# Kernel tuning notes

Measured on AMD Instinct MI355X. Metric: run time of the kernel, lower is better.

The kernel has to match this reference:

```python
import jax, jax.numpy as jnp
import numpy as np

CROP_SIZE = (14, 14)
NUM_LEVELS = 5
CANONICAL_SIZE = 224.0
CANONICAL_LEVEL = 1.0
EPS = 1e-7  # keras.backend.epsilon()


def _map_to_level(boxes):
    # boxes: [N, 4] (x1, y1, x2, y2) in image pixels
    w = boxes[:, 2] - boxes[:, 0]
    h = boxes[:, 3] - boxes[:, 1]
    size = jnp.sqrt(w * h)
    lv = jnp.floor(CANONICAL_LEVEL + jnp.log2(size / CANONICAL_SIZE + EPS))
    return jnp.clip(lv, 0.0, NUM_LEVELS - 1.0)


def _crop_and_resize(img, boxes, crop_size):
    # TF tf.image.crop_and_resize semantics (bilinear, extrapolation_value=0).
    # img: [H, W, C]; boxes: [N, 4] normalized (y1, x1, y2, x2)
    H, W, _ = img.shape
    ch, cw = crop_size
    y1, x1, y2, x2 = boxes[:, 0], boxes[:, 1], boxes[:, 2], boxes[:, 3]
    ty = jnp.arange(ch, dtype=boxes.dtype) / (ch - 1)
    tx = jnp.arange(cw, dtype=boxes.dtype) / (cw - 1)
    ys = (y1[:, None] * (1 - ty) + y2[:, None] * ty) * (H - 1)  # [N, ch]
    xs = (x1[:, None] * (1 - tx) + x2[:, None] * tx) * (W - 1)  # [N, cw]

    def corners(c, size):
        lo = jnp.floor(c)
        frac = c - lo
        lo_i = jnp.clip(lo, 0, size - 1).astype(jnp.int32)
        hi_i = jnp.clip(lo + 1, 0, size - 1).astype(jnp.int32)
        valid = (c >= 0) & (c <= size - 1)
        return lo_i, hi_i, frac, valid

    y0, y1i, fy, vy = corners(ys, H)
    x0, x1i, fx, vx = corners(xs, W)
    # gather 4 corners: [N, ch, cw, C]
    tl = img[y0[:, :, None], x0[:, None, :]]
    tr = img[y0[:, :, None], x1i[:, None, :]]
    bl = img[y1i[:, :, None], x0[:, None, :]]
    br = img[y1i[:, :, None], x1i[:, None, :]]
    fxb = fx[:, None, :, None]
    fyb = fy[:, :, None, None]
    top = tl + (tr - tl) * fxb
    bot = bl + (br - bl) * fxb
    out = top + (bot - top) * fyb
    mask = (vy[:, :, None] & vx[:, None, :])[:, :, :, None]
    return jnp.where(mask, out, 0.0)


def _roi_align(image_shape, boxes, scores, fpn):
    img_h = image_shape[1].astype(jnp.float32)
    img_w = image_shape[2].astype(jnp.float32)
    levels = _map_to_level(boxes)
    x1b, y1b, x2b, y2b = boxes[:, 0], boxes[:, 1], boxes[:, 2], boxes[:, 3]
    out = jnp.zeros((boxes.shape[0], CROP_SIZE[0], CROP_SIZE[1], fpn[0].shape[-1]),
                    dtype=fpn[0].dtype)
    for i, f in enumerate(fpn):
        fh = jnp.float32(f.shape[0])
        fw = jnp.float32(f.shape[1])
        # exact box normalization from the keras module
        nb = jnp.stack([
            y1b / img_h * fh / (fh - 1),
            x1b / img_w * fw / (fw - 1),
            (y2b / img_h * fh - 1) / (fh - 1),
            (x2b / img_w * fw - 1) / (fw - 1)], axis=1)
        crop = _crop_and_resize(f, nb, CROP_SIZE)
        sel = (levels == i)[:, None, None, None]
        # per-box level routing (equivalent to gather -> crop -> scatter_nd)
        out = out + jnp.where(sel, crop, 0.0)
    return out[None]  # [1, N, ch, cw, C]


def setup_inputs() -> dict:
    key = jax.random.key(0)
    ks = jax.random.split(key, 10)
    N, C, IMG = 512, 256, 1024.0
    cx = jax.random.uniform(ks[0], (N,), minval=16.0, maxval=IMG - 16.0)
    cy = jax.random.uniform(ks[1], (N,), minval=16.0, maxval=IMG - 16.0)
    # log-uniform box sizes 16..512 px so all 5 FPN levels are populated
    sz = jnp.exp(jax.random.uniform(ks[2], (N,), minval=jnp.log(16.0), maxval=jnp.log(512.0)))
    ar = jnp.exp(jax.random.uniform(ks[3], (N,), minval=jnp.log(0.5), maxval=jnp.log(2.0)))
    w = sz * jnp.sqrt(ar)
    h = sz / jnp.sqrt(ar)
    x1 = jnp.clip(cx - w / 2, 0.0, IMG)
    x2 = jnp.clip(cx + w / 2, 0.0, IMG)
    y1 = jnp.clip(cy - h / 2, 0.0, IMG)
    y2 = jnp.clip(cy + h / 2, 0.0, IMG)
    boxes = jnp.stack([x1, y1, x2, y2], axis=1)[None]  # [1, N, 4]
    scores = jax.random.uniform(ks[4], (1, N), dtype=jnp.float32)
    sizes = [256, 128, 64, 32, 16]  # FPN strides 4..64 on a 1024px image
    fpn = {f"fpn{i}": jax.random.normal(ks[5 + i], (1, s, s, C), dtype=jnp.float32)
           for i, s in enumerate(sizes)}
    return {"image_shape": jnp.array([1, 1024, 1024, 3], dtype=jnp.int32),
            "boxes": boxes, "scores": scores, **fpn}


def reference(image_shape, boxes, scores, fpn0, fpn1, fpn2, fpn3, fpn4):
    b = jax.lax.stop_gradient(boxes[0])
    s = jax.lax.stop_gradient(scores[0])
    fpn = [jax.lax.stop_gradient(f[0]) for f in (fpn0, fpn1, fpn2, fpn3, fpn4)]
    return _roi_align(image_shape, b, s, fpn)
```

## Files before the change

kernel.cpp:

```cpp
#include <hip/hip_runtime.h>


#define CROP 14
#define POS (CROP * CROP)
#define C 256
#define CANON 224.0f
#define EPSF 1e-7f
#define PPW 4
#define BLK_PER_BOX 13

typedef float vfloat4 __attribute__((ext_vector_type(4)));

__global__ __launch_bounds__(256) void roi_align_kernel(
    const int* __restrict__ image_shape,
    const float* __restrict__ boxes,
    const float* __restrict__ f0,
    const float* __restrict__ f1,
    const float* __restrict__ f2,
    const float* __restrict__ f3,
    const float* __restrict__ f4,
    float* __restrict__ out)
{
    const int nwg = gridDim.x;
    const int q = nwg >> 3, r = nwg & 7;
    const int xcd = blockIdx.x & 7, slot = blockIdx.x >> 3;
    const int blk = (xcd < r ? xcd * (q + 1) : r * (q + 1) + (xcd - r) * q) + slot;

    const int box      = blk / BLK_PER_BOX;
    const int blkInBox = blk % BLK_PER_BOX;
    const int wave = threadIdx.x >> 6;
    const int lane = threadIdx.x & 63;
    const int pbase = (blkInBox * 4 + wave) * PPW;

    const float imgh = (float)image_shape[1];
    const float imgw = (float)image_shape[2];

    const float bx1 = boxes[box * 4 + 0];
    const float by1 = boxes[box * 4 + 1];
    const float bx2 = boxes[box * 4 + 2];
    const float by2 = boxes[box * 4 + 3];

    const float w  = bx2 - bx1;
    const float h  = by2 - by1;
    const float sz = sqrtf(w * h);
    float lvf = floorf(1.0f + log2f(sz / CANON + EPSF));
    lvf = fminf(fmaxf(lvf, 0.0f), 4.0f);
    const int lv = (int)lvf;

    const int   s  = 256 >> lv;
    const float fh = (float)s;
    const float fw = (float)s;

    const float ny1 = by1 / imgh * fh / (fh - 1.0f);
    const float nx1 = bx1 / imgw * fw / (fw - 1.0f);
    const float ny2 = (by2 / imgh * fh - 1.0f) / (fh - 1.0f);
    const float nx2 = (bx2 / imgw * fw - 1.0f) / (fw - 1.0f);

    const float* __restrict__ f =
        (lv == 0) ? f0 : (lv == 1) ? f1 : (lv == 2) ? f2 : (lv == 3) ? f3 : f4;

    const int cbase = lane * 4;

    float  fxs[PPW], fys[PPW];
    bool   vv[PPW], act[PPW];
    size_t oTL[PPW], oTR[PPW], oBL[PPW], oBR[PPW];

    #pragma unroll
    for (int k = 0; k < PPW; ++k) {
        const int p  = pbase + k;
        act[k] = (p < POS);
        const int py = p / CROP;
        const int px = p % CROP;
        const float ty = (float)py / (float)(CROP - 1);
        const float tx = (float)px / (float)(CROP - 1);
        const float yc = (ny1 * (1.0f - ty) + ny2 * ty) * (fh - 1.0f);
        const float xc = (nx1 * (1.0f - tx) + nx2 * tx) * (fw - 1.0f);

        const float ylo = floorf(yc);
        fys[k] = yc - ylo;
        const int y0  = (int)fminf(fmaxf(ylo,        0.0f), fh - 1.0f);
        const int y1i = (int)fminf(fmaxf(ylo + 1.0f, 0.0f), fh - 1.0f);
        const bool vy = (yc >= 0.0f) && (yc <= fh - 1.0f);

        const float xlo = floorf(xc);
        fxs[k] = xc - xlo;
        const int x0  = (int)fminf(fmaxf(xlo,        0.0f), fw - 1.0f);
        const int x1i = (int)fminf(fmaxf(xlo + 1.0f, 0.0f), fw - 1.0f);
        const bool vx = (xc >= 0.0f) && (xc <= fw - 1.0f);

        vv[k] = vy && vx;
        oTL[k] = ((size_t)y0  * s + x0 ) * C + cbase;
        oTR[k] = ((size_t)y0  * s + x1i) * C + cbase;
        oBL[k] = ((size_t)y1i * s + x0 ) * C + cbase;
        oBR[k] = ((size_t)y1i * s + x1i) * C + cbase;
    }

    vfloat4 rTL[PPW], rTR[PPW], rBL[PPW], rBR[PPW];
    #pragma unroll
    for (int k = 0; k < PPW; ++k) {
        if (act[k]) {
            rTL[k] = *(const vfloat4*)(f + oTL[k]);
            rTR[k] = *(const vfloat4*)(f + oTR[k]);
            rBL[k] = *(const vfloat4*)(f + oBL[k]);
            rBR[k] = *(const vfloat4*)(f + oBR[k]);
        }
    }

    #pragma unroll
    for (int k = 0; k < PPW; ++k) {
        if (act[k]) {
            vfloat4 o;
            if (vv[k]) {
                const float fx = fxs[k], fy = fys[k];
                vfloat4 top = rTL[k] + (rTR[k] - rTL[k]) * fx;
                vfloat4 bot = rBL[k] + (rBR[k] - rBL[k]) * fx;
                o = top + (bot - top) * fy;
            } else { o = (vfloat4)0.0f; }
            vfloat4* dst = (vfloat4*)(out + ((size_t)box * POS + (pbase + k)) * C + cbase);
            __builtin_nontemporal_store(o, dst);
        }
    }
}

extern "C" void kernel_launch(void* const* d_in, const int* in_sizes, int n_in,
                              void* d_out, int out_size, void* d_ws, size_t ws_size,
                              hipStream_t stream) {
    const int*   image_shape = (const int*)d_in[0];
    const float* boxes       = (const float*)d_in[1];
    const float* f0 = (const float*)d_in[3];
    const float* f1 = (const float*)d_in[4];
    const float* f2 = (const float*)d_in[5];
    const float* f3 = (const float*)d_in[6];
    const float* f4 = (const float*)d_in[7];
    float* out = (float*)d_out;

    const int N = in_sizes[1] / 4;

    dim3 grid(N * BLK_PER_BOX);
    dim3 block(256);
    roi_align_kernel<<<grid, block, 0, stream>>>(
        image_shape, boxes, f0, f1, f2, f3, f4, out);
}
```

Baseline: 53.60 us.

## Split ROI align into setup and gather kernels via workspace records

Adds a setup kernel that computes, for every (box, sample position), the four corner offsets, the bilinear fractions, the level and a validity flag, and writes them to the workspace. A second gather kernel then reads one record per position and does only the four vector loads, the lerp and the store. It uses 2 positions per wave, so boxes no longer straddle blocks with idle tail lanes. The intent is to strip the per-block box and level arithmetic from the bandwidth-bound gather and balance the work. In exchange it adds a second launch and extra workspace traffic. A fallback monolithic kernel with 25 blocks per box runs when the workspace is too small.

```diff
diff --git a/kernel.cpp b/kernel.cpp
--- a/kernel.cpp
+++ b/kernel.cpp
@@ -6,12 +6,125 @@
 #define C 256
 #define CANON 224.0f
 #define EPSF 1e-7f
-#define PPW 4
-#define BLK_PER_BOX 13
 
 typedef float vfloat4 __attribute__((ext_vector_type(4)));
 
-__global__ __launch_bounds__(256) void roi_align_kernel(
+struct __align__(16) Rec {
+    int   off[4];
+    float fx, fy;
+    int   meta;
+    int   pad;
+};
+
+__global__ __launch_bounds__(256) void setup_kernel(
+    const int* __restrict__ image_shape,
+    const float* __restrict__ boxes,
+    Rec* __restrict__ recs,
+    int total)
+{
+    const int idx = blockIdx.x * 256 + threadIdx.x;
+    if (idx >= total) return;
+    const int box = idx / POS;
+    const int p   = idx % POS;
+    const int py  = p / CROP;
+    const int px  = p % CROP;
+
+    const float imgh = (float)image_shape[1];
+    const float imgw = (float)image_shape[2];
+
+    const float bx1 = boxes[box * 4 + 0];
+    const float by1 = boxes[box * 4 + 1];
+    const float bx2 = boxes[box * 4 + 2];
+    const float by2 = boxes[box * 4 + 3];
+
+    const float w  = bx2 - bx1;
+    const float h  = by2 - by1;
+    const float sz = sqrtf(w * h);
+    float lvf = floorf(1.0f + log2f(sz / CANON + EPSF));
+    lvf = fminf(fmaxf(lvf, 0.0f), 4.0f);
+    const int lv = (int)lvf;
+
+    const int   s  = 256 >> lv;
+    const float fh = (float)s;
+    const float fw = (float)s;
+
+    const float ny1 = by1 / imgh * fh / (fh - 1.0f);
+    const float nx1 = bx1 / imgw * fw / (fw - 1.0f);
+    const float ny2 = (by2 / imgh * fh - 1.0f) / (fh - 1.0f);
+    const float nx2 = (bx2 / imgw * fw - 1.0f) / (fw - 1.0f);
+
+    const float ty = (float)py / (float)(CROP - 1);
+    const float tx = (float)px / (float)(CROP - 1);
+    const float yc = (ny1 * (1.0f - ty) + ny2 * ty) * (fh - 1.0f);
+    const float xc = (nx1 * (1.0f - tx) + nx2 * tx) * (fw - 1.0f);
+
+    const float ylo = floorf(yc);
+    const float fy  = yc - ylo;
+    const int y0  = (int)fminf(fmaxf(ylo,        0.0f), fh - 1.0f);
+    const int y1i = (int)fminf(fmaxf(ylo + 1.0f, 0.0f), fh - 1.0f);
+    const bool vy = (yc >= 0.0f) && (yc <= fh - 1.0f);
+
+    const float xlo = floorf(xc);
+    const float fx  = xc - xlo;
+    const int x0  = (int)fminf(fmaxf(xlo,        0.0f), fw - 1.0f);
+    const int x1i = (int)fminf(fmaxf(xlo + 1.0f, 0.0f), fw - 1.0f);
+    const bool vx = (xc >= 0.0f) && (xc <= fw - 1.0f);
+
+    Rec r;
+    r.off[0] = (y0  * s + x0 ) * C;
+    r.off[1] = (y0  * s + x1i) * C;
+    r.off[2] = (y1i * s + x0 ) * C;
+    r.off[3] = (y1i * s + x1i) * C;
+    r.fx = fx; r.fy = fy;
+    r.meta = lv | ((vy && vx) ? 8 : 0);
+    r.pad = 0;
+    recs[idx] = r;
+}
+
+__global__ __launch_bounds__(256) void roi_gather_kernel(
+    const Rec* __restrict__ recs,
+    const float* __restrict__ f0,
+    const float* __restrict__ f1,
+    const float* __restrict__ f2,
+    const float* __restrict__ f3,
+    const float* __restrict__ f4,
+    float* __restrict__ out)
+{
+    const int nwg = gridDim.x;
+    const int q = nwg >> 3, r = nwg & 7;
+    const int xcd = blockIdx.x & 7, slot = blockIdx.x >> 3;
+    const int blk = (xcd < r ? xcd * (q + 1) : r * (q + 1) + (xcd - r) * q) + slot;
+
+    const int wave = threadIdx.x >> 6;
+    const int lane = threadIdx.x & 63;
+    const int g0 = blk * 8 + wave * 2;
+    const int cbase = lane * 4;
+
+    #pragma unroll
+    for (int k = 0; k < 2; ++k) {
+        const int g = g0 + k;
+        const Rec rec = recs[g];
+        const int lv = rec.meta & 7;
+        const float* __restrict__ f =
+            (lv == 0) ? f0 : (lv == 1) ? f1 : (lv == 2) ? f2 : (lv == 3) ? f3 : f4;
+
+        vfloat4 o;
+        if (rec.meta & 8) {
+            const vfloat4 tl = *(const vfloat4*)(f + rec.off[0] + cbase);
+            const vfloat4 tr = *(const vfloat4*)(f + rec.off[1] + cbase);
+            const vfloat4 bl = *(const vfloat4*)(f + rec.off[2] + cbase);
+            const vfloat4 br = *(const vfloat4*)(f + rec.off[3] + cbase);
+            const vfloat4 top = tl + (tr - tl) * rec.fx;
+            const vfloat4 bot = bl + (br - bl) * rec.fx;
+            o = top + (bot - top) * rec.fy;
+        } else {
+            o = (vfloat4)0.0f;
+        }
+        __builtin_nontemporal_store(o, (vfloat4*)(out + (size_t)g * C + cbase));
+    }
+}
+
+__global__ __launch_bounds__(256) void roi_align_mono(
     const int* __restrict__ image_shape,
     const float* __restrict__ boxes,
     const float* __restrict__ f0,
@@ -26,15 +139,14 @@
     const int xcd = blockIdx.x & 7, slot = blockIdx.x >> 3;
     const int blk = (xcd < r ? xcd * (q + 1) : r * (q + 1) + (xcd - r) * q) + slot;
 
-    const int box      = blk / BLK_PER_BOX;
-    const int blkInBox = blk % BLK_PER_BOX;
+    const int box      = blk / 25;
+    const int blkInBox = blk % 25;
     const int wave = threadIdx.x >> 6;
     const int lane = threadIdx.x & 63;
-    const int pbase = (blkInBox * 4 + wave) * PPW;
+    const int p0 = blkInBox * 8 + wave * 2;
 
     const float imgh = (float)image_shape[1];
     const float imgw = (float)image_shape[2];
-
     const float bx1 = boxes[box * 4 + 0];
     const float by1 = boxes[box * 4 + 1];
     const float bx2 = boxes[box * 4 + 2];
@@ -58,17 +170,12 @@
 
     const float* __restrict__ f =
         (lv == 0) ? f0 : (lv == 1) ? f1 : (lv == 2) ? f2 : (lv == 3) ? f3 : f4;
-
     const int cbase = lane * 4;
 
-    float  fxs[PPW], fys[PPW];
-    bool   vv[PPW], act[PPW];
-    size_t oTL[PPW], oTR[PPW], oBL[PPW], oBR[PPW];
-
     #pragma unroll
-    for (int k = 0; k < PPW; ++k) {
-        const int p  = pbase + k;
-        act[k] = (p < POS);
+    for (int k = 0; k < 2; ++k) {
+        const int p = p0 + k;
+        if (p >= POS) continue;
         const int py = p / CROP;
         const int px = p % CROP;
         const float ty = (float)py / (float)(CROP - 1);
@@ -77,48 +184,29 @@
         const float xc = (nx1 * (1.0f - tx) + nx2 * tx) * (fw - 1.0f);
 
         const float ylo = floorf(yc);
-        fys[k] = yc - ylo;
+        const float fy  = yc - ylo;
         const int y0  = (int)fminf(fmaxf(ylo,        0.0f), fh - 1.0f);
         const int y1i = (int)fminf(fmaxf(ylo + 1.0f, 0.0f), fh - 1.0f);
         const bool vy = (yc >= 0.0f) && (yc <= fh - 1.0f);
 
         const float xlo = floorf(xc);
-        fxs[k] = xc - xlo;
+        const float fx  = xc - xlo;
         const int x0  = (int)fminf(fmaxf(xlo,        0.0f), fw - 1.0f);
         const int x1i = (int)fminf(fmaxf(xlo + 1.0f, 0.0f), fw - 1.0f);
         const bool vx = (xc >= 0.0f) && (xc <= fw - 1.0f);
 
-        vv[k] = vy && vx;
-        oTL[k] = ((size_t)y0  * s + x0 ) * C + cbase;
-        oTR[k] = ((size_t)y0  * s + x1i) * C + cbase;
-        oBL[k] = ((size_t)y1i * s + x0 ) * C + cbase;
-        oBR[k] = ((size_t)y1i * s + x1i) * C + cbase;
-    }
-
-    vfloat4 rTL[PPW], rTR[PPW], rBL[PPW], rBR[PPW];
-    #pragma unroll
-    for (int k = 0; k < PPW; ++k) {
-        if (act[k]) {
-            rTL[k] = *(const vfloat4*)(f + oTL[k]);
-            rTR[k] = *(const vfloat4*)(f + oTR[k]);
-            rBL[k] = *(const vfloat4*)(f + oBL[k]);
-            rBR[k] = *(const vfloat4*)(f + oBR[k]);
-        }
-    }
-
-    #pragma unroll
-    for (int k = 0; k < PPW; ++k) {
-        if (act[k]) {
-            vfloat4 o;
-            if (vv[k]) {
-                const float fx = fxs[k], fy = fys[k];
-                vfloat4 top = rTL[k] + (rTR[k] - rTL[k]) * fx;
-                vfloat4 bot = rBL[k] + (rBR[k] - rBL[k]) * fx;
-                o = top + (bot - top) * fy;
-            } else { o = (vfloat4)0.0f; }
-            vfloat4* dst = (vfloat4*)(out + ((size_t)box * POS + (pbase + k)) * C + cbase);
-            __builtin_nontemporal_store(o, dst);
-        }
+        vfloat4 o;
+        if (vy && vx) {
+            const vfloat4 tl = *(const vfloat4*)(f + ((size_t)y0  * s + x0 ) * C + cbase);
+            const vfloat4 tr = *(const vfloat4*)(f + ((size_t)y0  * s + x1i) * C + cbase);
+            const vfloat4 bl = *(const vfloat4*)(f + ((size_t)y1i * s + x0 ) * C + cbase);
+            const vfloat4 br = *(const vfloat4*)(f + ((size_t)y1i * s + x1i) * C + cbase);
+            const vfloat4 top = tl + (tr - tl) * fx;
+            const vfloat4 bot = bl + (br - bl) * fx;
+            o = top + (bot - top) * fy;
+        } else { o = (vfloat4)0.0f; }
+        __builtin_nontemporal_store(
+            o, (vfloat4*)(out + ((size_t)box * POS + p) * C + cbase));
     }
 }
 
@@ -135,9 +223,17 @@
     float* out = (float*)d_out;
 
     const int N = in_sizes[1] / 4;
-
-    dim3 grid(N * BLK_PER_BOX);
-    dim3 block(256);
-    roi_align_kernel<<<grid, block, 0, stream>>>(
-        image_shape, boxes, f0, f1, f2, f3, f4, out);
-}
+    const int total = N * POS;
+    const size_t rec_bytes = (size_t)total * sizeof(Rec);
+
+    if (ws_size >= rec_bytes && (total % 8) == 0) {
+        Rec* recs = (Rec*)d_ws;
+        setup_kernel<<<(total + 255) / 256, 256, 0, stream>>>(
+            image_shape, boxes, recs, total);
+        roi_gather_kernel<<<total / 8, 256, 0, stream>>>(
+            recs, f0, f1, f2, f3, f4, out);
+    } else {
+        roi_align_mono<<<N * 25, 256, 0, stream>>>(
+            image_shape, boxes, f0, f1, f2, f3, f4, out);
+    }
+}
```

New measurement: 56.69 us. 1.06x slower.

## Halve positions per wave, skip loads for invalid points, use inline-asm bypass stores

Applied to the files above, without the earlier changes.

Each wave now handles 2 crop positions instead of 4, so the grid grows from 13 to 25 blocks per box and more waves run in parallel. Corner loads are issued only for sample points that fall inside the feature map, which avoids gathers whose results would be zeroed anyway. Output stores use inline-asm global_store_dwordx4 with sc0 sc1 nt cache bits instead of the nontemporal builtin. Each wave has fewer loads in flight, and the loads now sit behind a branch, which may reduce memory-level parallelism per wave.

```diff
diff --git a/kernel.cpp b/kernel.cpp
--- a/kernel.cpp
+++ b/kernel.cpp
@@ -6,10 +6,15 @@
 #define C 256
 #define CANON 224.0f
 #define EPSF 1e-7f
-#define PPW 4
-#define BLK_PER_BOX 13
 
 typedef float vfloat4 __attribute__((ext_vector_type(4)));
+
+__device__ __forceinline__ void store_bypass(float* p, vfloat4 v) {
+    asm volatile("global_store_dwordx4 %0, %1, off sc0 sc1 nt"
+                 :
+                 : "v"(p), "v"(v)
+                 : "memory");
+}
 
 __global__ __launch_bounds__(256) void roi_align_kernel(
     const int* __restrict__ image_shape,
@@ -26,15 +31,14 @@
     const int xcd = blockIdx.x & 7, slot = blockIdx.x >> 3;
     const int blk = (xcd < r ? xcd * (q + 1) : r * (q + 1) + (xcd - r) * q) + slot;
 
-    const int box      = blk / BLK_PER_BOX;
-    const int blkInBox = blk % BLK_PER_BOX;
+    const int box      = blk / 25;
+    const int blkInBox = blk % 25;
     const int wave = threadIdx.x >> 6;
     const int lane = threadIdx.x & 63;
-    const int pbase = (blkInBox * 4 + wave) * PPW;
+    const int p0 = blkInBox * 8 + wave * 2;
 
     const float imgh = (float)image_shape[1];
     const float imgw = (float)image_shape[2];
-
     const float bx1 = boxes[box * 4 + 0];
     const float by1 = boxes[box * 4 + 1];
     const float bx2 = boxes[box * 4 + 2];
@@ -58,17 +62,12 @@
 
     const float* __restrict__ f =
         (lv == 0) ? f0 : (lv == 1) ? f1 : (lv == 2) ? f2 : (lv == 3) ? f3 : f4;
-
     const int cbase = lane * 4;
 
-    float  fxs[PPW], fys[PPW];
-    bool   vv[PPW], act[PPW];
-    size_t oTL[PPW], oTR[PPW], oBL[PPW], oBR[PPW];
-
     #pragma unroll
-    for (int k = 0; k < PPW; ++k) {
-        const int p  = pbase + k;
-        act[k] = (p < POS);
+    for (int k = 0; k < 2; ++k) {
+        const int p = p0 + k;
+        if (p >= POS) continue;
         const int py = p / CROP;
         const int px = p % CROP;
         const float ty = (float)py / (float)(CROP - 1);
@@ -77,48 +76,29 @@
         const float xc = (nx1 * (1.0f - tx) + nx2 * tx) * (fw - 1.0f);
 
         const float ylo = floorf(yc);
-        fys[k] = yc - ylo;
+        const float fy  = yc - ylo;
         const int y0  = (int)fminf(fmaxf(ylo,        0.0f), fh - 1.0f);
         const int y1i = (int)fminf(fmaxf(ylo + 1.0f, 0.0f), fh - 1.0f);
         const bool vy = (yc >= 0.0f) && (yc <= fh - 1.0f);
 
         const float xlo = floorf(xc);
-        fxs[k] = xc - xlo;
+        const float fx  = xc - xlo;
         const int x0  = (int)fminf(fmaxf(xlo,        0.0f), fw - 1.0f);
         const int x1i = (int)fminf(fmaxf(xlo + 1.0f, 0.0f), fw - 1.0f);
         const bool vx = (xc >= 0.0f) && (xc <= fw - 1.0f);
 
-        vv[k] = vy && vx;
-        oTL[k] = ((size_t)y0  * s + x0 ) * C + cbase;
-        oTR[k] = ((size_t)y0  * s + x1i) * C + cbase;
-        oBL[k] = ((size_t)y1i * s + x0 ) * C + cbase;
-        oBR[k] = ((size_t)y1i * s + x1i) * C + cbase;
-    }
+        vfloat4 o;
+        if (vy && vx) {
+            const vfloat4 tl = *(const vfloat4*)(f + ((size_t)y0  * s + x0 ) * C + cbase);
+            const vfloat4 tr = *(const vfloat4*)(f + ((size_t)y0  * s + x1i) * C + cbase);
+            const vfloat4 bl = *(const vfloat4*)(f + ((size_t)y1i * s + x0 ) * C + cbase);
+            const vfloat4 br = *(const vfloat4*)(f + ((size_t)y1i * s + x1i) * C + cbase);
+            const vfloat4 top = tl + (tr - tl) * fx;
+            const vfloat4 bot = bl + (br - bl) * fx;
+            o = top + (bot - top) * fy;
+        } else { o = (vfloat4)0.0f; }
 
-    vfloat4 rTL[PPW], rTR[PPW], rBL[PPW], rBR[PPW];
-    #pragma unroll
-    for (int k = 0; k < PPW; ++k) {
-        if (act[k]) {
-            rTL[k] = *(const vfloat4*)(f + oTL[k]);
-            rTR[k] = *(const vfloat4*)(f + oTR[k]);
-            rBL[k] = *(const vfloat4*)(f + oBL[k]);
-            rBR[k] = *(const vfloat4*)(f + oBR[k]);
-        }
-    }
-
-    #pragma unroll
-    for (int k = 0; k < PPW; ++k) {
-        if (act[k]) {
-            vfloat4 o;
-            if (vv[k]) {
-                const float fx = fxs[k], fy = fys[k];
-                vfloat4 top = rTL[k] + (rTR[k] - rTL[k]) * fx;
-                vfloat4 bot = rBL[k] + (rBR[k] - rBL[k]) * fx;
-                o = top + (bot - top) * fy;
-            } else { o = (vfloat4)0.0f; }
-            vfloat4* dst = (vfloat4*)(out + ((size_t)box * POS + (pbase + k)) * C + cbase);
-            __builtin_nontemporal_store(o, dst);
-        }
+        store_bypass(out + ((size_t)box * POS + p) * C + cbase, o);
     }
 }
 
@@ -136,8 +116,6 @@
 
     const int N = in_sizes[1] / 4;
 
-    dim3 grid(N * BLK_PER_BOX);
-    dim3 block(256);
-    roi_align_kernel<<<grid, block, 0, stream>>>(
+    roi_align_kernel<<<N * 25, 256, 0, stream>>>(
         image_shape, boxes, f0, f1, f2, f3, f4, out);
 }
```

Result: faster. 52.14 us (median of 2 runs) (-2.7%).
